# Kernel optimization log

Measured on AMD Instinct MI355X. Metric: run time of the kernel, lower is better.

## Reference

```python
import jax, jax.numpy as jnp
import numpy as np

# ---- static problem dims (mirror the Triton kernel's constexprs) ----
NUM_SEQS = 2
LQ = 1024            # query tokens per sequence (uniform varlen instance)
HIST = 1024          # cached-prefix length per sequence
LK = LQ + HIST       # total kv length per sequence
NUM_HEADS = 32
NUM_KV_HEADS = 8
HEAD_DIM = 128
BLOCK_SIZE = 64
MAX_NUM_BLOCKS = LK // BLOCK_SIZE          # 32 logical blocks per sequence
TOTAL_BLOCKS = NUM_SEQS * MAX_NUM_BLOCKS   # physical blocks in the cache
NEG = -1e10                                # matches kernel's -10000000000.0


def setup_inputs() -> dict:
    key = jax.random.key(0)
    k1, k2, k3, k4 = jax.random.split(key, 4)
    q = jax.random.normal(k1, (NUM_SEQS * LQ, NUM_HEADS, HEAD_DIM), jnp.float32)
    k_cache = jax.random.normal(k2, (TOTAL_BLOCKS, BLOCK_SIZE, NUM_KV_HEADS, HEAD_DIM), jnp.float32)
    v_cache = jax.random.normal(k3, (TOTAL_BLOCKS, BLOCK_SIZE, NUM_KV_HEADS, HEAD_DIM), jnp.float32)
    cu_seqlens_q = (jnp.arange(NUM_SEQS + 1, dtype=jnp.int32) * LQ)
    cu_seqlens_k = (jnp.arange(NUM_SEQS + 1, dtype=jnp.int32) * LK)
    # scattered physical block layout: a random permutation -> irregular gather
    block_tables = jax.random.permutation(k4, TOTAL_BLOCKS).astype(jnp.int32).reshape(NUM_SEQS, MAX_NUM_BLOCKS)
    return dict(q=q, k_cache=k_cache, v_cache=v_cache,
                cu_seqlens_q=cu_seqlens_q, cu_seqlens_k=cu_seqlens_k,
                block_tables=block_tables)


def _paged_prefill_attention(q, k_cache, v_cache, cu_seqlens_q, cu_seqlens_k, block_tables):
    scale = 1.0 / np.sqrt(HEAD_DIM)
    seq_len_q = cu_seqlens_q[1:] - cu_seqlens_q[:-1]            # [S]
    seq_len_k = cu_seqlens_k[1:] - cu_seqlens_k[:-1]            # [S]
    history_len = seq_len_k - seq_len_q                          # [S]

    # uniform varlen instance: flat [total_q, H, D] -> [S, LQ, H, D]
    qr = q.reshape(NUM_SEQS, LQ, NUM_HEADS, HEAD_DIM)
    group = NUM_HEADS // NUM_KV_HEADS
    # [S, LQ, KVH, G, D] so head h maps to kv head h // group (kernel's kv_head_idx)
    q5 = qr.reshape(NUM_SEQS, LQ, NUM_KV_HEADS, group, HEAD_DIM) * scale

    # block-table gather: logical kv layout per sequence
    safe_tables = jnp.maximum(block_tables, 0)
    k = k_cache[safe_tables].reshape(NUM_SEQS, LK, NUM_KV_HEADS, HEAD_DIM)
    v = v_cache[safe_tables].reshape(NUM_SEQS, LK, NUM_KV_HEADS, HEAD_DIM)

    # scores [S, KVH, G, LQ, LK]
    scores = jnp.einsum('sqhgd,skhd->shgqk', q5, k)

    pos_q = jnp.arange(LQ, dtype=jnp.int32)[None, :] + history_len[:, None]   # [S, LQ] absolute positions
    pos_k = jnp.arange(LK, dtype=jnp.int32)                                   # [LK]
    valid_k = (pos_k[None, :] < seq_len_k[:, None]) & \
              jnp.repeat(block_tables >= 0, BLOCK_SIZE, axis=1)               # [S, LK]
    causal = pos_q[:, :, None] >= pos_k[None, None, :]                        # [S, LQ, LK]
    mask = causal & valid_k[:, None, :]
    scores = jnp.where(mask[:, None, None, :, :], scores, NEG)

    p = jax.nn.softmax(scores, axis=-1)  # online-softmax in kernel == exact softmax
    out = jnp.einsum('shgqk,skhd->sqhgd', p, v)
    return out.reshape(NUM_SEQS * LQ, NUM_HEADS, HEAD_DIM)


def reference(q, k_cache, v_cache, cu_seqlens_q, cu_seqlens_k, block_tables):
    return _paged_prefill_attention(q, k_cache, v_cache, cu_seqlens_q, cu_seqlens_k, block_tables)
```

## Files before the change

### kernel.cpp

```cpp
#include <hip/hip_runtime.h>
#include <hip/hip_bf16.h>

#define NS_    2
#define LQ_    1024
#define HIST_  1024
#define LK_    2048
#define NH_    32
#define NKVH_  8
#define HD_    128
#define BS_    64
#define BM_    128
#define MAXB_  32

typedef __attribute__((ext_vector_type(8))) short short8;
typedef __attribute__((ext_vector_type(4))) float f32x4;

#define VSTR 72

static __device__ __forceinline__ unsigned short f2bf(float x) {
    __hip_bfloat16 h = __float2bfloat16(x);
    return *(unsigned short*)&h;
}

static __device__ __forceinline__ void cp16(const void* g, void* l) {
    __builtin_amdgcn_global_load_lds(
        (const __attribute__((address_space(1))) void*)g,
        (__attribute__((address_space(3))) void*)l, 16, 0, 0);
}

template<int CTRL>
static __device__ __forceinline__ float dppmax(float x) {
    int y = __builtin_amdgcn_update_dpp(0, __float_as_int(x), CTRL, 0xf, 0xf, true);
    return fmaxf(x, __int_as_float(y));
}

__global__ __launch_bounds__(256)
void prep_kv(const float* __restrict__ kc, const float* __restrict__ vc,
             const int* __restrict__ bt,
             unsigned short* __restrict__ Kb, unsigned short* __restrict__ Vb)
{
    __shared__ __align__(16) unsigned short Vt[HD_ * VSTR];
    const int tid = threadIdx.x;
    const int gid = blockIdx.x;
    const int seq = gid >> 8;
    const int kvh = (gid >> 5) & 7;
    const int blk = gid & 31;
    const int ph  = bt[seq * MAXB_ + blk];
    const size_t src = ((size_t)ph * BS_ * NKVH_ + kvh) * HD_;
    const int grp = seq * NKVH_ + kvh;
    const int t8 = tid >> 5, q32 = tid & 31;

    float4 kr[8], vr[8];
#pragma unroll
    for (int p = 0; p < 8; ++p)
        kr[p] = *(const float4*)(kc + src + (size_t)(p * 8 + t8) * (NKVH_ * HD_) + q32 * 4);
#pragma unroll
    for (int j = 0; j < 8; ++j)
        vr[j] = *(const float4*)(vc + src + (size_t)(t8 * 8 + j) * (NKVH_ * HD_) + q32 * 4);

#pragma unroll
    for (int p = 0; p < 8; ++p) {
        unsigned short u[4] = {f2bf(kr[p].x), f2bf(kr[p].y), f2bf(kr[p].z), f2bf(kr[p].w)};
        *(uint2*)(Kb + ((size_t)grp * LK_ + blk * BS_ + p * 8 + t8) * HD_ + q32 * 4) = *(const uint2*)u;
    }
#pragma unroll
    for (int w2 = 0; w2 < 4; ++w2) {
        unsigned short row[8];
#pragma unroll
        for (int j = 0; j < 8; ++j) {
            float f = (w2 == 0) ? vr[j].x : (w2 == 1) ? vr[j].y : (w2 == 2) ? vr[j].z : vr[j].w;
            row[j] = f2bf(f);
        }
        *(short8*)&Vt[(q32 * 4 + w2) * VSTR + t8 * 8] = *(const short8*)row;
    }
    __syncthreads();
#pragma unroll
    for (int u = 0; u < 4; ++u) {
        const int c  = tid + 256 * u;
        const int d  = c >> 3, ch = c & 7;
        uint4 x = *(const uint4*)&Vt[d * VSTR + ch * 8];
        *(uint4*)(Vb + ((size_t)grp * HD_ + d) * LK_ + blk * BS_ + ch * 8) = x;
    }
}

template<bool PREP>
__global__ __launch_bounds__(256, 2)
void paged_attn(const float* __restrict__ q,
                const unsigned short* __restrict__ Kb,
                const unsigned short* __restrict__ Vb,
                const float* __restrict__ kc,
                const float* __restrict__ vc,
                const int* __restrict__ bt,
                float* __restrict__ out)
{
    __shared__ __align__(16) unsigned short Ksh[2][BS_ * HD_];
    __shared__ __align__(16) unsigned short Vsh[2][HD_ * BS_];
    __shared__ __align__(16) unsigned short Psh[BM_ * BS_];

    const int tid  = threadIdx.x;
    const int w    = tid >> 6;
    const int lane = tid & 63;
    const int n    = lane & 15;
    const int q4   = lane >> 4;

    const int gid  = blockIdx.x;
    const int kvh  = gid & 7;
    const int slot = gid >> 3;
    const int seq  = slot >> 5;
    const int sub  = slot & 31;
    const int e    = sub & 1;
    const int t3   = (sub >> 1) & 7;
    const int hp   = sub >> 4;
    const int head = kvh * 4 + hp * 2 + e;
    const int m0   = (e ? (7 - t3) : t3) * BM_;
    const int r0   = m0 + w * 32;
    const int grp  = seq * NKVH_ + kvh;

    const float SC = 0.08838834764831845f * 1.4426950408889634f;
    short8 qf[2][4];
#pragma unroll
    for (int rt = 0; rt < 2; ++rt) {
        const size_t base = ((size_t)((seq * LQ_ + r0 + rt * 16 + n) * NH_ + head)) * HD_;
#pragma unroll
        for (int c = 0; c < 4; ++c) {
            float4 a = *(const float4*)(q + base + c * 32 + q4 * 8);
            float4 b = *(const float4*)(q + base + c * 32 + q4 * 8 + 4);
            unsigned short u[8] = {f2bf(a.x * SC), f2bf(a.y * SC), f2bf(a.z * SC), f2bf(a.w * SC),
                                   f2bf(b.x * SC), f2bf(b.y * SC), f2bf(b.z * SC), f2bf(b.w * SC)};
            qf[rt][c] = *(const short8*)u;
        }
    }

    f32x4 acc[2][8];
    f32x4 lf[2];
    float mrow[2][4];
#pragma unroll
    for (int rt = 0; rt < 2; ++rt) {
        lf[rt] = (f32x4){0.f, 0.f, 0.f, 0.f};
#pragma unroll
        for (int dt = 0; dt < 8; ++dt) acc[rt][dt] = (f32x4){0.f, 0.f, 0.f, 0.f};
#pragma unroll
        for (int r = 0; r < 4; ++r) mrow[rt][r] = -1e30f;
    }

    const int nb = (HIST_ + m0 + BM_ - 1) / BS_ + 1;
    const unsigned short* kSrc = Kb + (size_t)grp * LK_ * HD_;
    const unsigned short* vSrc = Vb + (size_t)grp * HD_ * LK_;

    const int krow_ = w * 16 + (lane >> 4);
    const int kc8_  = ((lane & 15) ^ (krow_ & 15));
    const int vd_   = w * 32 + (lane >> 3);
    const int vc8_  = ((lane & 7) ^ (vd_ & 7));

    auto issue = [&](int b, int buf) {
#pragma unroll
        for (int j = 0; j < 4; ++j) {
            const int row = krow_ + j * 4;
            const int c8  = (lane & 15) ^ (row & 15);
            cp16(kSrc + ((size_t)b * BS_ + row) * HD_ + c8 * 8, &Ksh[buf][(w * 16 + j * 4) * HD_]);
        }
#pragma unroll
        for (int j = 0; j < 4; ++j) {
            const int d  = vd_ + j * 8;
            const int c8 = (lane & 7) ^ (d & 7);
            cp16(vSrc + (size_t)d * LK_ + b * BS_ + c8 * 8, &Vsh[buf][(w * 32 + j * 8) * BS_]);
        }
    };

    if constexpr (PREP) issue(0, 0);
    short8 ones;
#pragma unroll
    for (int j = 0; j < 8; ++j) ones[j] = (short)0x3F80;

    for (int b = 0; b < nb; ++b) {
        const int cur = PREP ? (b & 1) : 0;
        __syncthreads();
        if constexpr (PREP) {
            if (b + 1 < nb) issue(b + 1, 1 ^ cur);
        } else {
            const int ph = bt[seq * MAXB_ + b];
            const size_t src = ((size_t)ph * BS_ * NKVH_ + kvh) * HD_;
#pragma unroll
            for (int j = 0; j < 4; ++j) {
                const int row = w * 16 + j * 4 + (lane >> 4);
                const int c8  = (lane & 15) ^ (row & 15);
                float4 a = *(const float4*)(kc + src + (size_t)row * (NKVH_ * HD_) + c8 * 8);
                float4 b2 = *(const float4*)(kc + src + (size_t)row * (NKVH_ * HD_) + c8 * 8 + 4);
                unsigned short u[8] = {f2bf(a.x), f2bf(a.y), f2bf(a.z), f2bf(a.w),
                                       f2bf(b2.x), f2bf(b2.y), f2bf(b2.z), f2bf(b2.w)};
                *(short8*)&Ksh[0][row * HD_ + (lane & 15) * 8] = *(const short8*)u;
            }
#pragma unroll
            for (int j = 0; j < 4; ++j) {
                const int d  = w * 32 + j * 8 + (lane >> 3);
                const int c8 = (lane & 7) ^ (d & 7);
                unsigned short u[8];
#pragma unroll
                for (int i2 = 0; i2 < 8; ++i2)
                    u[i2] = f2bf(vc[src + (size_t)(c8 * 8 + i2) * (NKVH_ * HD_) + d]);
                *(short8*)&Vsh[0][d * BS_ + (lane & 7) * 8] = *(const short8*)u;
            }
            __syncthreads();
        }

        if (64 * b <= HIST_ + r0 + 31) {
            f32x4 s[2][4];
#pragma unroll
            for (int rt = 0; rt < 2; ++rt)
#pragma unroll
                for (int kt = 0; kt < 4; ++kt) s[rt][kt] = (f32x4){0.f, 0.f, 0.f, 0.f};
#pragma unroll
            for (int kt = 0; kt < 4; ++kt) {
#pragma unroll
                for (int c = 0; c < 4; ++c) {
                    short8 kf = *(const short8*)&Ksh[cur][(kt * 16 + n) * HD_ + (((c * 4 + q4) ^ n) << 3)];
#pragma unroll
                    for (int rt = 0; rt < 2; ++rt)
                        s[rt][kt] = __builtin_amdgcn_mfma_f32_16x16x32_bf16(qf[rt][c], kf, s[rt][kt], 0, 0, 0);
                }
            }
            const bool needMask = (64 * b + 63 > HIST_ + r0);
#pragma unroll
            for (int rt = 0; rt < 2; ++rt) {
                float mx[4], al[4];
#pragma unroll
                for (int r = 0; r < 4; ++r) mx[r] = -1e30f;
#pragma unroll
                for (int kt = 0; kt < 4; ++kt) {
#pragma unroll
                    for (int r = 0; r < 4; ++r) {
                        float t = s[rt][kt][r];
                        if (needMask) {
                            const int key = b * 64 + kt * 16 + n;
                            const int row = r0 + rt * 16 + q4 * 4 + r;
                            if (key > HIST_ + row) t = -1e30f;
                        }
                        s[rt][kt][r] = t;
                        mx[r] = fmaxf(mx[r], t);
                    }
                }
#pragma unroll
                for (int r = 0; r < 4; ++r) {
                    mx[r] = dppmax<0xB1>(mx[r]);
                    mx[r] = dppmax<0x4E>(mx[r]);
                    mx[r] = dppmax<0x124>(mx[r]);
                    mx[r] = dppmax<0x128>(mx[r]);
                    const float mn = fmaxf(mrow[rt][r], mx[r]);
                    al[r] = __builtin_amdgcn_exp2f(mrow[rt][r] - mn);
                    mrow[rt][r] = mn;
                }
                const int rbase = w * 32 + rt * 16 + q4 * 4;
#pragma unroll
                for (int kt = 0; kt < 4; ++kt) {
                    const int cb = kt * 2 + (n >> 3);
                    const int ci = n & 7;
#pragma unroll
                    for (int r = 0; r < 4; ++r) {
                        const int row = rbase + r;
                        const float p = __builtin_amdgcn_exp2f(s[rt][kt][r] - mrow[rt][r]);
                        Psh[row * BS_ + ((cb ^ (row & 7)) << 3) + ci] = f2bf(p);
                    }
                }
                if (__any(al[0] != 1.f || al[1] != 1.f || al[2] != 1.f || al[3] != 1.f)) {
#pragma unroll
                    for (int dt = 0; dt < 8; ++dt)
#pragma unroll
                        for (int r = 0; r < 4; ++r) acc[rt][dt][r] *= al[r];
#pragma unroll
                    for (int r = 0; r < 4; ++r) lf[rt][r] *= al[r];
                }
            }
#pragma unroll
            for (int ks = 0; ks < 2; ++ks) {
                short8 pa[2];
#pragma unroll
                for (int rt = 0; rt < 2; ++rt)
                    pa[rt] = *(const short8*)&Psh[(w * 32 + rt * 16 + n) * BS_ + (((ks * 4 + q4) ^ (n & 7)) << 3)];
#pragma unroll
                for (int rt = 0; rt < 2; ++rt)
                    lf[rt] = __builtin_amdgcn_mfma_f32_16x16x32_bf16(pa[rt], ones, lf[rt], 0, 0, 0);
#pragma unroll
                for (int dt = 0; dt < 8; ++dt) {
                    short8 vf = *(const short8*)&Vsh[cur][(dt * 16 + n) * BS_ + (((ks * 4 + q4) ^ (n & 7)) << 3)];
#pragma unroll
                    for (int rt = 0; rt < 2; ++rt)
                        acc[rt][dt] = __builtin_amdgcn_mfma_f32_16x16x32_bf16(pa[rt], vf, acc[rt][dt], 0, 0, 0);
                }
            }
        }
    }

#pragma unroll
    for (int rt = 0; rt < 2; ++rt) {
        float rl[4];
#pragma unroll
        for (int r = 0; r < 4; ++r) rl[r] = 1.0f / lf[rt][r];
#pragma unroll
        for (int dt = 0; dt < 8; ++dt)
#pragma unroll
            for (int r = 0; r < 4; ++r) {
                const int row = r0 + rt * 16 + q4 * 4 + r;
                out[((size_t)((seq * LQ_ + row) * NH_ + head)) * HD_ + dt * 16 + n] = acc[rt][dt][r] * rl[r];
            }
    }
}

extern "C" void kernel_launch(void* const* d_in, const int* in_sizes, int n_in,
                              void* d_out, int out_size, void* d_ws, size_t ws_size,
                              hipStream_t stream) {
    const float* q  = (const float*)d_in[0];
    const float* kc = (const float*)d_in[1];
    const float* vc = (const float*)d_in[2];
    const int*   bt = (const int*)d_in[5];
    float*      out = (float*)d_out;
    (void)in_sizes; (void)n_in; (void)out_size;

    const size_t kb_elems = (size_t)NS_ * NKVH_ * LK_ * HD_;
    const size_t need = kb_elems * 2 * sizeof(unsigned short);
    if (ws_size >= need) {
        unsigned short* Kb = (unsigned short*)d_ws;
        unsigned short* Vb = Kb + kb_elems;
        prep_kv<<<512, 256, 0, stream>>>(kc, vc, bt, Kb, Vb);
        paged_attn<true><<<512, 256, 0, stream>>>(q, Kb, Vb, kc, vc, bt, out);
    } else {
        paged_attn<false><<<512, 256, 0, stream>>>(q, nullptr, nullptr, kc, vc, bt, out);
    }
}
```

Before: 208.3 us.

## Use 8 waves of 16 query rows per block and raise MFMA priority

Each 128-row query tile is now split across 8 wavefronts of 16 rows each instead of 4 wavefronts of 32 rows, so block size goes from 256 to 512 threads and per-thread accumulator registers are halved. Tile loads are redistributed so each wave copies half as many K/V rows. s_setprio is raised around the MFMA sections so matrix work is scheduled ahead of other waves. The aim is more resident waves per CU and better latency hiding. The trade-off is that each K/V fragment read from LDS is reused for only one row tile instead of two, which doubles LDS read traffic per MFMA.

```diff
diff --git a/kernel.cpp b/kernel.cpp
--- a/kernel.cpp
+++ b/kernel.cpp
@@ -84,7 +84,7 @@
 }
 
 template<bool PREP>
-__global__ __launch_bounds__(256, 2)
+__global__ __launch_bounds__(512, 4)
 void paged_attn(const float* __restrict__ q,
                 const unsigned short* __restrict__ Kb,
                 const unsigned short* __restrict__ Vb,
@@ -113,57 +113,47 @@
     const int hp   = sub >> 4;
     const int head = kvh * 4 + hp * 2 + e;
     const int m0   = (e ? (7 - t3) : t3) * BM_;
-    const int r0   = m0 + w * 32;
+    const int r0   = m0 + w * 16;
     const int grp  = seq * NKVH_ + kvh;
 
     const float SC = 0.08838834764831845f * 1.4426950408889634f;
-    short8 qf[2][4];
-#pragma unroll
-    for (int rt = 0; rt < 2; ++rt) {
-        const size_t base = ((size_t)((seq * LQ_ + r0 + rt * 16 + n) * NH_ + head)) * HD_;
+    short8 qf[4];
+    {
+        const size_t base = ((size_t)((seq * LQ_ + r0 + n) * NH_ + head)) * HD_;
 #pragma unroll
         for (int c = 0; c < 4; ++c) {
             float4 a = *(const float4*)(q + base + c * 32 + q4 * 8);
             float4 b = *(const float4*)(q + base + c * 32 + q4 * 8 + 4);
             unsigned short u[8] = {f2bf(a.x * SC), f2bf(a.y * SC), f2bf(a.z * SC), f2bf(a.w * SC),
                                    f2bf(b.x * SC), f2bf(b.y * SC), f2bf(b.z * SC), f2bf(b.w * SC)};
-            qf[rt][c] = *(const short8*)u;
-        }
-    }
-
-    f32x4 acc[2][8];
-    f32x4 lf[2];
-    float mrow[2][4];
-#pragma unroll
-    for (int rt = 0; rt < 2; ++rt) {
-        lf[rt] = (f32x4){0.f, 0.f, 0.f, 0.f};
-#pragma unroll
-        for (int dt = 0; dt < 8; ++dt) acc[rt][dt] = (f32x4){0.f, 0.f, 0.f, 0.f};
-#pragma unroll
-        for (int r = 0; r < 4; ++r) mrow[rt][r] = -1e30f;
-    }
+            qf[c] = *(const short8*)u;
+        }
+    }
+
+    f32x4 acc[8];
+    f32x4 lf = (f32x4){0.f, 0.f, 0.f, 0.f};
+    float mrow[4];
+#pragma unroll
+    for (int dt = 0; dt < 8; ++dt) acc[dt] = (f32x4){0.f, 0.f, 0.f, 0.f};
+#pragma unroll
+    for (int r = 0; r < 4; ++r) mrow[r] = -1e30f;
 
     const int nb = (HIST_ + m0 + BM_ - 1) / BS_ + 1;
     const unsigned short* kSrc = Kb + (size_t)grp * LK_ * HD_;
     const unsigned short* vSrc = Vb + (size_t)grp * HD_ * LK_;
 
-    const int krow_ = w * 16 + (lane >> 4);
-    const int kc8_  = ((lane & 15) ^ (krow_ & 15));
-    const int vd_   = w * 32 + (lane >> 3);
-    const int vc8_  = ((lane & 7) ^ (vd_ & 7));
-
     auto issue = [&](int b, int buf) {
 #pragma unroll
-        for (int j = 0; j < 4; ++j) {
-            const int row = krow_ + j * 4;
+        for (int j = 0; j < 2; ++j) {
+            const int row = w * 8 + j * 4 + (lane >> 4);
             const int c8  = (lane & 15) ^ (row & 15);
-            cp16(kSrc + ((size_t)b * BS_ + row) * HD_ + c8 * 8, &Ksh[buf][(w * 16 + j * 4) * HD_]);
-        }
-#pragma unroll
-        for (int j = 0; j < 4; ++j) {
-            const int d  = vd_ + j * 8;
+            cp16(kSrc + ((size_t)b * BS_ + row) * HD_ + c8 * 8, &Ksh[buf][(w * 8 + j * 4) * HD_]);
+        }
+#pragma unroll
+        for (int j = 0; j < 2; ++j) {
+            const int d  = w * 16 + j * 8 + (lane >> 3);
             const int c8 = (lane & 7) ^ (d & 7);
-            cp16(vSrc + (size_t)d * LK_ + b * BS_ + c8 * 8, &Vsh[buf][(w * 32 + j * 8) * BS_]);
+            cp16(vSrc + (size_t)d * LK_ + b * BS_ + c8 * 8, &Vsh[buf][(w * 16 + j * 8) * BS_]);
         }
     };
 
@@ -181,8 +171,8 @@
             const int ph = bt[seq * MAXB_ + b];
             const size_t src = ((size_t)ph * BS_ * NKVH_ + kvh) * HD_;
 #pragma unroll
-            for (int j = 0; j < 4; ++j) {
-                const int row = w * 16 + j * 4 + (lane >> 4);
+            for (int j = 0; j < 2; ++j) {
+                const int row = w * 8 + j * 4 + (lane >> 4);
                 const int c8  = (lane & 15) ^ (row & 15);
                 float4 a = *(const float4*)(kc + src + (size_t)row * (NKVH_ * HD_) + c8 * 8);
                 float4 b2 = *(const float4*)(kc + src + (size_t)row * (NKVH_ * HD_) + c8 * 8 + 4);
@@ -191,8 +181,8 @@
                 *(short8*)&Ksh[0][row * HD_ + (lane & 15) * 8] = *(const short8*)u;
             }
 #pragma unroll
-            for (int j = 0; j < 4; ++j) {
-                const int d  = w * 32 + j * 8 + (lane >> 3);
+            for (int j = 0; j < 2; ++j) {
+                const int d  = w * 16 + j * 8 + (lane >> 3);
                 const int c8 = (lane & 7) ^ (d & 7);
                 unsigned short u[8];
 #pragma unroll
@@ -203,104 +193,94 @@
             __syncthreads();
         }
 
-        if (64 * b <= HIST_ + r0 + 31) {
-            f32x4 s[2][4];
-#pragma unroll
-            for (int rt = 0; rt < 2; ++rt)
-#pragma unroll
-                for (int kt = 0; kt < 4; ++kt) s[rt][kt] = (f32x4){0.f, 0.f, 0.f, 0.f};
+        if (64 * b <= HIST_ + r0 + 15) {
+            f32x4 s[4];
+#pragma unroll
+            for (int kt = 0; kt < 4; ++kt) s[kt] = (f32x4){0.f, 0.f, 0.f, 0.f};
+            __builtin_amdgcn_s_setprio(1);
 #pragma unroll
             for (int kt = 0; kt < 4; ++kt) {
 #pragma unroll
                 for (int c = 0; c < 4; ++c) {
                     short8 kf = *(const short8*)&Ksh[cur][(kt * 16 + n) * HD_ + (((c * 4 + q4) ^ n) << 3)];
-#pragma unroll
-                    for (int rt = 0; rt < 2; ++rt)
-                        s[rt][kt] = __builtin_amdgcn_mfma_f32_16x16x32_bf16(qf[rt][c], kf, s[rt][kt], 0, 0, 0);
+                    s[kt] = __builtin_amdgcn_mfma_f32_16x16x32_bf16(qf[c], kf, s[kt], 0, 0, 0);
                 }
             }
+            __builtin_amdgcn_s_setprio(0);
+
             const bool needMask = (64 * b + 63 > HIST_ + r0);
-#pragma unroll
-            for (int rt = 0; rt < 2; ++rt) {
-                float mx[4], al[4];
-#pragma unroll
-                for (int r = 0; r < 4; ++r) mx[r] = -1e30f;
-#pragma unroll
-                for (int kt = 0; kt < 4; ++kt) {
-#pragma unroll
-                    for (int r = 0; r < 4; ++r) {
-                        float t = s[rt][kt][r];
-                        if (needMask) {
-                            const int key = b * 64 + kt * 16 + n;
-                            const int row = r0 + rt * 16 + q4 * 4 + r;
-                            if (key > HIST_ + row) t = -1e30f;
-                        }
-                        s[rt][kt][r] = t;
-                        mx[r] = fmaxf(mx[r], t);
+            float mx[4], al[4];
+#pragma unroll
+            for (int r = 0; r < 4; ++r) mx[r] = -1e30f;
+#pragma unroll
+            for (int kt = 0; kt < 4; ++kt) {
+#pragma unroll
+                for (int r = 0; r < 4; ++r) {
+                    float t = s[kt][r];
+                    if (needMask) {
+                        const int key = b * 64 + kt * 16 + n;
+                        const int row = r0 + q4 * 4 + r;
+                        if (key > HIST_ + row) t = -1e30f;
                     }
+                    s[kt][r] = t;
+                    mx[r] = fmaxf(mx[r], t);
                 }
+            }
+#pragma unroll
+            for (int r = 0; r < 4; ++r) {
+                mx[r] = dppmax<0xB1>(mx[r]);
+                mx[r] = dppmax<0x4E>(mx[r]);
+                mx[r] = dppmax<0x124>(mx[r]);
+                mx[r] = dppmax<0x128>(mx[r]);
+                const float mn = fmaxf(mrow[r], mx[r]);
+                al[r] = __builtin_amdgcn_exp2f(mrow[r] - mn);
+                mrow[r] = mn;
+            }
+            const int rbase = w * 16 + q4 * 4;
+#pragma unroll
+            for (int kt = 0; kt < 4; ++kt) {
+                const int cb = kt * 2 + (n >> 3);
+                const int ci = n & 7;
 #pragma unroll
                 for (int r = 0; r < 4; ++r) {
-                    mx[r] = dppmax<0xB1>(mx[r]);
-                    mx[r] = dppmax<0x4E>(mx[r]);
-                    mx[r] = dppmax<0x124>(mx[r]);
-                    mx[r] = dppmax<0x128>(mx[r]);
-                    const float mn = fmaxf(mrow[rt][r], mx[r]);
-                    al[r] = __builtin_amdgcn_exp2f(mrow[rt][r] - mn);
-                    mrow[rt][r] = mn;
+                    const int row = rbase + r;
+                    const float p = __builtin_amdgcn_exp2f(s[kt][r] - mrow[r]);
+                    Psh[row * BS_ + ((cb ^ (row & 7)) << 3) + ci] = f2bf(p);
                 }
-                const int rbase = w * 32 + rt * 16 + q4 * 4;
-#pragma unroll
-                for (int kt = 0; kt < 4; ++kt) {
-                    const int cb = kt * 2 + (n >> 3);
-                    const int ci = n & 7;
-#pragma unroll
-                    for (int r = 0; r < 4; ++r) {
-                        const int row = rbase + r;
-                        const float p = __builtin_amdgcn_exp2f(s[rt][kt][r] - mrow[rt][r]);
-                        Psh[row * BS_ + ((cb ^ (row & 7)) << 3) + ci] = f2bf(p);
-                    }
-                }
-                if (__any(al[0] != 1.f || al[1] != 1.f || al[2] != 1.f || al[3] != 1.f)) {
-#pragma unroll
-                    for (int dt = 0; dt < 8; ++dt)
-#pragma unroll
-                        for (int r = 0; r < 4; ++r) acc[rt][dt][r] *= al[r];
-#pragma unroll
-                    for (int r = 0; r < 4; ++r) lf[rt][r] *= al[r];
-                }
-            }
+            }
+            if (__any(al[0] != 1.f || al[1] != 1.f || al[2] != 1.f || al[3] != 1.f)) {
+#pragma unroll
+                for (int dt = 0; dt < 8; ++dt)
+#pragma unroll
+                    for (int r = 0; r < 4; ++r) acc[dt][r] *= al[r];
+#pragma unroll
+                for (int r = 0; r < 4; ++r) lf[r] *= al[r];
+            }
+            __builtin_amdgcn_s_setprio(1);
 #pragma unroll
             for (int ks = 0; ks < 2; ++ks) {
-                short8 pa[2];
-#pragma unroll
-                for (int rt = 0; rt < 2; ++rt)
-                    pa[rt] = *(const short8*)&Psh[(w * 32 + rt * 16 + n) * BS_ + (((ks * 4 + q4) ^ (n & 7)) << 3)];
-#pragma unroll
-                for (int rt = 0; rt < 2; ++rt)
-                    lf[rt] = __builtin_amdgcn_mfma_f32_16x16x32_bf16(pa[rt], ones, lf[rt], 0, 0, 0);
+                short8 pa = *(const short8*)&Psh[(w * 16 + n) * BS_ + (((ks * 4 + q4) ^ (n & 7)) << 3)];
+                lf = __builtin_amdgcn_mfma_f32_16x16x32_bf16(pa, ones, lf, 0, 0, 0);
 #pragma unroll
                 for (int dt = 0; dt < 8; ++dt) {
                     short8 vf = *(const short8*)&Vsh[cur][(dt * 16 + n) * BS_ + (((ks * 4 + q4) ^ (n & 7)) << 3)];
-#pragma unroll
-                    for (int rt = 0; rt < 2; ++rt)
-                        acc[rt][dt] = __builtin_amdgcn_mfma_f32_16x16x32_bf16(pa[rt], vf, acc[rt][dt], 0, 0, 0);
+                    acc[dt] = __builtin_amdgcn_mfma_f32_16x16x32_bf16(pa, vf, acc[dt], 0, 0, 0);
                 }
             }
-        }
-    }
-
-#pragma unroll
-    for (int rt = 0; rt < 2; ++rt) {
+            __builtin_amdgcn_s_setprio(0);
+        }
+    }
+
+    {
         float rl[4];
 #pragma unroll
-        for (int r = 0; r < 4; ++r) rl[r] = 1.0f / lf[rt][r];
+        for (int r = 0; r < 4; ++r) rl[r] = 1.0f / lf[r];
 #pragma unroll
         for (int dt = 0; dt < 8; ++dt)
 #pragma unroll
             for (int r = 0; r < 4; ++r) {
-                const int row = r0 + rt * 16 + q4 * 4 + r;
-                out[((size_t)((seq * LQ_ + row) * NH_ + head)) * HD_ + dt * 16 + n] = acc[rt][dt][r] * rl[r];
+                const int row = r0 + q4 * 4 + r;
+                out[((size_t)((seq * LQ_ + row) * NH_ + head)) * HD_ + dt * 16 + n] = acc[dt][r] * rl[r];
             }
     }
 }
@@ -321,8 +301,8 @@
         unsigned short* Kb = (unsigned short*)d_ws;
         unsigned short* Vb = Kb + kb_elems;
         prep_kv<<<512, 256, 0, stream>>>(kc, vc, bt, Kb, Vb);
-        paged_attn<true><<<512, 256, 0, stream>>>(q, Kb, Vb, kc, vc, bt, out);
+        paged_attn<true><<<512, 512, 0, stream>>>(q, Kb, Vb, kc, vc, bt, out);
     } else {
-        paged_attn<false><<<512, 256, 0, stream>>>(q, nullptr, nullptr, kc, vc, bt, out);
-    }
-}
+        paged_attn<false><<<512, 512, 0, stream>>>(q, nullptr, nullptr, kc, vc, bt, out);
+    }
+}
```

Result: faster. 202.6 us (-2.7%).

## Split each KV block across two wave groups with a final softmax merge

Applied to the files above, without the earlier changes.

Each workgroup now has 512 threads instead of 256. Eight waves split each 64-key block into two 32-key halves: four row groups times two key halves, each holding separate running max/sum/accumulator state. At the end, the second half's partial results go through shared memory (reusing the K/V/P buffers) and are merged into the first half with a log-sum-exp rescale. The aim is more waves per CU, and so more latency hiding, at the cost of an extra merge pass and more shared-memory traffic. s_setprio hints are also added around the MFMA sections.

```diff
diff --git a/kernel.cpp b/kernel.cpp
--- a/kernel.cpp
+++ b/kernel.cpp
@@ -84,7 +84,7 @@
 }
 
 template<bool PREP>
-__global__ __launch_bounds__(256, 2)
+__global__ __launch_bounds__(512, 4)
 void paged_attn(const float* __restrict__ q,
                 const unsigned short* __restrict__ Kb,
                 const unsigned short* __restrict__ Vb,
@@ -102,6 +102,8 @@
     const int lane = tid & 63;
     const int n    = lane & 15;
     const int q4   = lane >> 4;
+    const int rg   = w & 3;
+    const int kh   = w >> 2;
 
     const int gid  = blockIdx.x;
     const int kvh  = gid & 7;
@@ -113,7 +115,7 @@
     const int hp   = sub >> 4;
     const int head = kvh * 4 + hp * 2 + e;
     const int m0   = (e ? (7 - t3) : t3) * BM_;
-    const int r0   = m0 + w * 32;
+    const int r0   = m0 + rg * 32;
     const int grp  = seq * NKVH_ + kvh;
 
     const float SC = 0.08838834764831845f * 1.4426950408889634f;
@@ -147,23 +149,18 @@
     const unsigned short* kSrc = Kb + (size_t)grp * LK_ * HD_;
     const unsigned short* vSrc = Vb + (size_t)grp * HD_ * LK_;
 
-    const int krow_ = w * 16 + (lane >> 4);
-    const int kc8_  = ((lane & 15) ^ (krow_ & 15));
-    const int vd_   = w * 32 + (lane >> 3);
-    const int vc8_  = ((lane & 7) ^ (vd_ & 7));
-
     auto issue = [&](int b, int buf) {
 #pragma unroll
-        for (int j = 0; j < 4; ++j) {
-            const int row = krow_ + j * 4;
+        for (int j = 0; j < 2; ++j) {
+            const int row = w * 8 + j * 4 + (lane >> 4);
             const int c8  = (lane & 15) ^ (row & 15);
-            cp16(kSrc + ((size_t)b * BS_ + row) * HD_ + c8 * 8, &Ksh[buf][(w * 16 + j * 4) * HD_]);
-        }
-#pragma unroll
-        for (int j = 0; j < 4; ++j) {
-            const int d  = vd_ + j * 8;
+            cp16(kSrc + ((size_t)b * BS_ + row) * HD_ + c8 * 8, &Ksh[buf][(w * 8 + j * 4) * HD_]);
+        }
+#pragma unroll
+        for (int j = 0; j < 2; ++j) {
+            const int d  = w * 16 + j * 8 + (lane >> 3);
             const int c8 = (lane & 7) ^ (d & 7);
-            cp16(vSrc + (size_t)d * LK_ + b * BS_ + c8 * 8, &Vsh[buf][(w * 32 + j * 8) * BS_]);
+            cp16(vSrc + (size_t)d * LK_ + b * BS_ + c8 * 8, &Vsh[buf][(w * 16 + j * 8) * BS_]);
         }
     };
 
@@ -181,8 +178,8 @@
             const int ph = bt[seq * MAXB_ + b];
             const size_t src = ((size_t)ph * BS_ * NKVH_ + kvh) * HD_;
 #pragma unroll
-            for (int j = 0; j < 4; ++j) {
-                const int row = w * 16 + j * 4 + (lane >> 4);
+            for (int j = 0; j < 2; ++j) {
+                const int row = w * 8 + j * 4 + (lane >> 4);
                 const int c8  = (lane & 15) ^ (row & 15);
                 float4 a = *(const float4*)(kc + src + (size_t)row * (NKVH_ * HD_) + c8 * 8);
                 float4 b2 = *(const float4*)(kc + src + (size_t)row * (NKVH_ * HD_) + c8 * 8 + 4);
@@ -191,8 +188,8 @@
                 *(short8*)&Ksh[0][row * HD_ + (lane & 15) * 8] = *(const short8*)u;
             }
 #pragma unroll
-            for (int j = 0; j < 4; ++j) {
-                const int d  = w * 32 + j * 8 + (lane >> 3);
+            for (int j = 0; j < 2; ++j) {
+                const int d  = w * 16 + j * 8 + (lane >> 3);
                 const int c8 = (lane & 7) ^ (d & 7);
                 unsigned short u[8];
 #pragma unroll
@@ -203,56 +200,64 @@
             __syncthreads();
         }
 
-        if (64 * b <= HIST_ + r0 + 31) {
-            f32x4 s[2][4];
-#pragma unroll
-            for (int rt = 0; rt < 2; ++rt)
-#pragma unroll
-                for (int kt = 0; kt < 4; ++kt) s[rt][kt] = (f32x4){0.f, 0.f, 0.f, 0.f};
-#pragma unroll
-            for (int kt = 0; kt < 4; ++kt) {
+        if (64 * b + kh * 32 <= HIST_ + r0 + 31) {
+            f32x4 s[2][2];
+#pragma unroll
+            for (int rt = 0; rt < 2; ++rt)
+#pragma unroll
+                for (int kt = 0; kt < 2; ++kt) s[rt][kt] = (f32x4){0.f, 0.f, 0.f, 0.f};
+            __builtin_amdgcn_s_setprio(1);
+#pragma unroll
+            for (int kt = 0; kt < 2; ++kt) {
 #pragma unroll
                 for (int c = 0; c < 4; ++c) {
-                    short8 kf = *(const short8*)&Ksh[cur][(kt * 16 + n) * HD_ + (((c * 4 + q4) ^ n) << 3)];
-#pragma unroll
-                    for (int rt = 0; rt < 2; ++rt)
-                        s[rt][kt] = __builtin_amdgcn_mfma_f32_16x16x32_bf16(qf[rt][c], kf, s[rt][kt], 0, 0, 0);
-                }
-            }
-            const bool needMask = (64 * b + 63 > HIST_ + r0);
-#pragma unroll
-            for (int rt = 0; rt < 2; ++rt) {
-                float mx[4], al[4];
-#pragma unroll
-                for (int r = 0; r < 4; ++r) mx[r] = -1e30f;
-#pragma unroll
-                for (int kt = 0; kt < 4; ++kt) {
+                    short8 kf = *(const short8*)&Ksh[cur][((kh * 2 + kt) * 16 + n) * HD_ + (((c * 4 + q4) ^ n) << 3)];
+                    s[0][kt] = __builtin_amdgcn_mfma_f32_16x16x32_bf16(qf[0][c], kf, s[0][kt], 0, 0, 0);
+                    s[1][kt] = __builtin_amdgcn_mfma_f32_16x16x32_bf16(qf[1][c], kf, s[1][kt], 0, 0, 0);
+                }
+            }
+            __builtin_amdgcn_s_setprio(0);
+
+            const bool needMask = (64 * b + kh * 32 + 31 > HIST_ + r0);
+            float mx[2][4], al[2][4];
+#pragma unroll
+            for (int rt = 0; rt < 2; ++rt)
+#pragma unroll
+                for (int r = 0; r < 4; ++r) mx[rt][r] = -1e30f;
+#pragma unroll
+            for (int rt = 0; rt < 2; ++rt)
+#pragma unroll
+                for (int kt = 0; kt < 2; ++kt)
 #pragma unroll
                     for (int r = 0; r < 4; ++r) {
                         float t = s[rt][kt][r];
                         if (needMask) {
-                            const int key = b * 64 + kt * 16 + n;
+                            const int key = b * 64 + kh * 32 + kt * 16 + n;
                             const int row = r0 + rt * 16 + q4 * 4 + r;
                             if (key > HIST_ + row) t = -1e30f;
                         }
                         s[rt][kt][r] = t;
-                        mx[r] = fmaxf(mx[r], t);
+                        mx[rt][r] = fmaxf(mx[rt][r], t);
                     }
-                }
+#pragma unroll
+            for (int rt = 0; rt < 2; ++rt)
 #pragma unroll
                 for (int r = 0; r < 4; ++r) {
-                    mx[r] = dppmax<0xB1>(mx[r]);
-                    mx[r] = dppmax<0x4E>(mx[r]);
-                    mx[r] = dppmax<0x124>(mx[r]);
-                    mx[r] = dppmax<0x128>(mx[r]);
-                    const float mn = fmaxf(mrow[rt][r], mx[r]);
-                    al[r] = __builtin_amdgcn_exp2f(mrow[rt][r] - mn);
+                    float m = mx[rt][r];
+                    m = dppmax<0xB1>(m);
+                    m = dppmax<0x4E>(m);
+                    m = dppmax<0x124>(m);
+                    m = dppmax<0x128>(m);
+                    const float mn = fmaxf(mrow[rt][r], m);
+                    al[rt][r] = __builtin_amdgcn_exp2f(mrow[rt][r] - mn);
                     mrow[rt][r] = mn;
                 }
-                const int rbase = w * 32 + rt * 16 + q4 * 4;
-#pragma unroll
-                for (int kt = 0; kt < 4; ++kt) {
-                    const int cb = kt * 2 + (n >> 3);
+#pragma unroll
+            for (int rt = 0; rt < 2; ++rt) {
+                const int rbase = rg * 32 + rt * 16 + q4 * 4;
+#pragma unroll
+                for (int kt = 0; kt < 2; ++kt) {
+                    const int cb = kh * 4 + kt * 2 + (n >> 3);
                     const int ci = n & 7;
 #pragma unroll
                     for (int r = 0; r < 4; ++r) {
@@ -261,47 +266,79 @@
                         Psh[row * BS_ + ((cb ^ (row & 7)) << 3) + ci] = f2bf(p);
                     }
                 }
-                if (__any(al[0] != 1.f || al[1] != 1.f || al[2] != 1.f || al[3] != 1.f)) {
+            }
+            if (__any(al[0][0] != 1.f || al[0][1] != 1.f || al[0][2] != 1.f || al[0][3] != 1.f ||
+                      al[1][0] != 1.f || al[1][1] != 1.f || al[1][2] != 1.f || al[1][3] != 1.f)) {
+#pragma unroll
+                for (int rt = 0; rt < 2; ++rt) {
 #pragma unroll
                     for (int dt = 0; dt < 8; ++dt)
 #pragma unroll
-                        for (int r = 0; r < 4; ++r) acc[rt][dt][r] *= al[r];
-#pragma unroll
-                    for (int r = 0; r < 4; ++r) lf[rt][r] *= al[r];
-                }
-            }
-#pragma unroll
-            for (int ks = 0; ks < 2; ++ks) {
-                short8 pa[2];
-#pragma unroll
-                for (int rt = 0; rt < 2; ++rt)
-                    pa[rt] = *(const short8*)&Psh[(w * 32 + rt * 16 + n) * BS_ + (((ks * 4 + q4) ^ (n & 7)) << 3)];
-#pragma unroll
-                for (int rt = 0; rt < 2; ++rt)
-                    lf[rt] = __builtin_amdgcn_mfma_f32_16x16x32_bf16(pa[rt], ones, lf[rt], 0, 0, 0);
-#pragma unroll
-                for (int dt = 0; dt < 8; ++dt) {
-                    short8 vf = *(const short8*)&Vsh[cur][(dt * 16 + n) * BS_ + (((ks * 4 + q4) ^ (n & 7)) << 3)];
-#pragma unroll
-                    for (int rt = 0; rt < 2; ++rt)
-                        acc[rt][dt] = __builtin_amdgcn_mfma_f32_16x16x32_bf16(pa[rt], vf, acc[rt][dt], 0, 0, 0);
-                }
-            }
-        }
-    }
-
-#pragma unroll
-    for (int rt = 0; rt < 2; ++rt) {
-        float rl[4];
-#pragma unroll
-        for (int r = 0; r < 4; ++r) rl[r] = 1.0f / lf[rt][r];
-#pragma unroll
-        for (int dt = 0; dt < 8; ++dt)
+                        for (int r = 0; r < 4; ++r) acc[rt][dt][r] *= al[rt][r];
+#pragma unroll
+                    for (int r = 0; r < 4; ++r) lf[rt][r] *= al[rt][r];
+                }
+            }
+            short8 pa[2];
+#pragma unroll
+            for (int rt = 0; rt < 2; ++rt)
+                pa[rt] = *(const short8*)&Psh[(rg * 32 + rt * 16 + n) * BS_ + (((kh * 4 + q4) ^ (n & 7)) << 3)];
+            __builtin_amdgcn_s_setprio(1);
+            lf[0] = __builtin_amdgcn_mfma_f32_16x16x32_bf16(pa[0], ones, lf[0], 0, 0, 0);
+            lf[1] = __builtin_amdgcn_mfma_f32_16x16x32_bf16(pa[1], ones, lf[1], 0, 0, 0);
+#pragma unroll
+            for (int dt = 0; dt < 8; ++dt) {
+                short8 vf = *(const short8*)&Vsh[cur][(dt * 16 + n) * BS_ + (((kh * 4 + q4) ^ (n & 7)) << 3)];
+                acc[0][dt] = __builtin_amdgcn_mfma_f32_16x16x32_bf16(pa[0], vf, acc[0][dt], 0, 0, 0);
+                acc[1][dt] = __builtin_amdgcn_mfma_f32_16x16x32_bf16(pa[1], vf, acc[1][dt], 0, 0, 0);
+            }
+            __builtin_amdgcn_s_setprio(0);
+        }
+    }
+
+    __syncthreads();
+    float* accS = (rg == 0) ? (float*)&Ksh[0][0] : (rg == 1) ? (float*)&Ksh[1][0]
+                : (rg == 2) ? (float*)&Vsh[0][0] : (float*)&Vsh[1][0];
+    float* mlS  = (float*)Psh + rg * 1024;
+    if (kh == 1) {
+#pragma unroll
+        for (int rt = 0; rt < 2; ++rt) {
+            *(f32x4*)&mlS[lane * 16 + rt * 4] =
+                (f32x4){mrow[rt][0], mrow[rt][1], mrow[rt][2], mrow[rt][3]};
+            *(f32x4*)&mlS[lane * 16 + 8 + rt * 4] = lf[rt];
+#pragma unroll
+            for (int dt = 0; dt < 8; ++dt) {
+                const int idx = rt * 8 + dt;
+                *(f32x4*)&accS[lane * 64 + ((idx ^ (lane & 15)) << 2)] = acc[rt][dt];
+            }
+        }
+    }
+    __syncthreads();
+    if (kh == 0) {
+#pragma unroll
+        for (int rt = 0; rt < 2; ++rt) {
+            f32x4 m1 = *(const f32x4*)&mlS[lane * 16 + rt * 4];
+            f32x4 l1 = *(const f32x4*)&mlS[lane * 16 + 8 + rt * 4];
+            float a0[4], a1[4], rl[4];
 #pragma unroll
             for (int r = 0; r < 4; ++r) {
-                const int row = r0 + rt * 16 + q4 * 4 + r;
-                out[((size_t)((seq * LQ_ + row) * NH_ + head)) * HD_ + dt * 16 + n] = acc[rt][dt][r] * rl[r];
-            }
+                const float M = fmaxf(mrow[rt][r], m1[r]);
+                a0[r] = __builtin_amdgcn_exp2f(mrow[rt][r] - M);
+                a1[r] = __builtin_amdgcn_exp2f(m1[r] - M);
+                rl[r] = 1.0f / (lf[rt][r] * a0[r] + l1[r] * a1[r]);
+            }
+#pragma unroll
+            for (int dt = 0; dt < 8; ++dt) {
+                const int idx = rt * 8 + dt;
+                f32x4 o1 = *(const f32x4*)&accS[lane * 64 + ((idx ^ (lane & 15)) << 2)];
+#pragma unroll
+                for (int r = 0; r < 4; ++r) {
+                    const int row = r0 + rt * 16 + q4 * 4 + r;
+                    out[((size_t)((seq * LQ_ + row) * NH_ + head)) * HD_ + dt * 16 + n] =
+                        (acc[rt][dt][r] * a0[r] + o1[r] * a1[r]) * rl[r];
+                }
+            }
+        }
     }
 }
 
@@ -321,8 +358,8 @@
         unsigned short* Kb = (unsigned short*)d_ws;
         unsigned short* Vb = Kb + kb_elems;
         prep_kv<<<512, 256, 0, stream>>>(kc, vc, bt, Kb, Vb);
-        paged_attn<true><<<512, 256, 0, stream>>>(q, Kb, Vb, kc, vc, bt, out);
+        paged_attn<true><<<512, 512, 0, stream>>>(q, Kb, Vb, kc, vc, bt, out);
     } else {
-        paged_attn<false><<<512, 256, 0, stream>>>(q, nullptr, nullptr, kc, vc, bt, out);
-    }
-}
+        paged_attn<false><<<512, 512, 0, stream>>>(q, nullptr, nullptr, kc, vc, bt, out);
+    }
+}
```

Result: slower. 543.8 us (+161.1%).
